# Kernel optimization log

Hardware: AMD Instinct MI355X
Metric: run time of the kernel (lower is better)

## Reference

```python
import jax, jax.numpy as jnp
import numpy as np

K = 3          # kernel size
PAD = 1        # padding


def _conv2d(x, w, b):
    # plain 3x3 conv, stride 1, pad 1, NCHW / OIHW
    out = jax.lax.conv_general_dilated(
        x, w, window_strides=(1, 1), padding=((PAD, PAD), (PAD, PAD)),
        dimension_numbers=('NCHW', 'OIHW', 'NCHW'))
    return out + b[None, :, None, None]


def _deform_conv2d(x, offsets, w, b):
    # torchvision deform_conv2d semantics (stride=1, dilation=1, no mask)
    B, C, H, W = x.shape
    K2 = K * K
    off = offsets.reshape(B, K2, 2, H, W)
    dy, dx = off[:, :, 0], off[:, :, 1]              # [B,K2,H,W], (y,x) order
    ki, kj = jnp.meshgrid(jnp.arange(K), jnp.arange(K), indexing='ij')
    ki = ki.reshape(K2).astype(x.dtype)
    kj = kj.reshape(K2).astype(x.dtype)
    base_y = (jnp.arange(H, dtype=x.dtype)[None, :, None] - PAD + ki[:, None, None])  # [K2,H,1]
    base_x = (jnp.arange(W, dtype=x.dtype)[None, None, :] - PAD + kj[:, None, None])  # [K2,1,W]
    py = base_y[None] + dy                            # [B,K2,H,W] sampling rows
    px = base_x[None] + dx                            # [B,K2,H,W] sampling cols

    y0 = jnp.floor(py); x0 = jnp.floor(px)
    y1 = y0 + 1.0;      x1 = x0 + 1.0
    wy1 = py - y0; wy0 = 1.0 - wy1
    wx1 = px - x0; wx0 = 1.0 - wx1

    def corner(yc, xc, wgt):
        valid = ((yc >= 0) & (yc <= H - 1) & (xc >= 0) & (xc <= W - 1))
        iy = jnp.clip(yc, 0, H - 1).astype(jnp.int32)
        ix = jnp.clip(xc, 0, W - 1).astype(jnp.int32)
        # per-batch gather: x[b][:, iy[b], ix[b]] -> [C,K2,H,W]
        vals = jax.vmap(lambda xb, iyb, ixb: xb[:, iyb, ixb])(x, iy, ix)
        return vals * (wgt * valid.astype(x.dtype))[:, None]  # [B,C,K2,H,W]

    sampled = (corner(y0, x0, wy0 * wx0) + corner(y0, x1, wy0 * wx1)
               + corner(y1, x0, wy1 * wx0) + corner(y1, x1, wy1 * wx1))
    out = jnp.einsum('bckhw,ock->bohw', sampled, w.reshape(w.shape[0], C, K2))
    return out + b[None, :, None, None]


def setup_inputs() -> dict:
    key = jax.random.key(0)
    ks = jax.random.split(key, 6)
    B, C, O, H, W = 4, 256, 256, 64, 64
    x = jax.random.normal(ks[0], (B, C, H, W), dtype=jnp.float32)
    y = jax.random.normal(ks[1], (B, C, H, W), dtype=jnp.float32)
    # offset conv predicts 2*K*K offset channels; small init keeps offsets a few px
    offset_w = jax.random.normal(ks[2], (2 * K * K, C, K, K), dtype=jnp.float32) * 0.01
    offset_b = jax.random.normal(ks[3], (2 * K * K,), dtype=jnp.float32) * 0.01
    deform_w = jax.random.normal(ks[4], (O, C, K, K), dtype=jnp.float32) * (1.0 / np.sqrt(C * K * K))
    deform_b = jax.random.normal(ks[5], (O,), dtype=jnp.float32) * 0.01
    return {"x": x, "y": y, "offset_w": offset_w, "offset_b": offset_b,
            "deform_w": deform_w, "deform_b": deform_b}


def reference(x, y, offset_w, offset_b, deform_w, deform_b):
    offsets = _conv2d(y, offset_w, offset_b)          # [B, 2*K*K, H, W]
    return _deform_conv2d(x, offsets, deform_w, deform_b)
```

## Files before the change

kernel.cpp:

```cpp
#include <hip/hip_runtime.h>
#include <hip/hip_bf16.h>
#include <stdint.h>


typedef __bf16 bf16x8 __attribute__((ext_vector_type(8)));
typedef float  f32x4  __attribute__((ext_vector_type(4)));

__device__ __forceinline__ unsigned short f2bfu(float f) {
    union { float f; unsigned u; } v; v.f = f;
    return (unsigned short)((v.u + 0x8000u) >> 16);
}
__device__ __forceinline__ float lo16(unsigned u) {
    union { unsigned u; float f; } v; v.u = u << 16; return v.f;
}
__device__ __forceinline__ float hi16(unsigned u) {
    union { unsigned u; float f; } v; v.u = u & 0xFFFF0000u; return v.f;
}
__device__ __forceinline__ unsigned fbits(float f) {
    union { float f; unsigned u; } v; v.f = f; return v.u;
}
__device__ __forceinline__ unsigned blend2(unsigned u0, unsigned u1, unsigned u2, unsigned u3,
                                           float4 w) {
    float lo = w.x * lo16(u0) + w.y * lo16(u1) + w.z * lo16(u2) + w.w * lo16(u3);
    float hi = w.x * hi16(u0) + w.y * hi16(u1) + w.z * hi16(u2) + w.w * hi16(u3);
    unsigned rl = fbits(lo) + 0x8000u;
    unsigned rh = fbits(hi) + 0x8000u;
    return __builtin_amdgcn_perm(rh, rl, 0x07060302);
}

__device__ __forceinline__ void wait_ge(int* f, int v) {
    while (__hip_atomic_load(f, __ATOMIC_ACQUIRE, __HIP_MEMORY_SCOPE_WORKGROUP) < v)
        __builtin_amdgcn_s_sleep(1);
}
__device__ __forceinline__ void signal_one(int* f, int lane) {
    __threadfence_block();
    if (lane == 0)
        __hip_atomic_fetch_add(f, 1, __ATOMIC_RELEASE, __HIP_MEMORY_SCOPE_WORKGROUP);
}

__global__ __launch_bounds__(256) void prep_kernel(
    const float* __restrict__ x, const float* __restrict__ y,
    const float* __restrict__ ow, const float* __restrict__ dw,
    unsigned short* __restrict__ xT, unsigned short* __restrict__ yT,
    unsigned short* __restrict__ Wp2, unsigned short* __restrict__ Bo)
{
    __shared__ float tile[64 * 69];
    int blk = blockIdx.x;
    int t = threadIdx.x;
    if (blk < 2048) {
        const float* src = x; unsigned short* dst = xT;
        if (blk >= 1024) { src = y; dst = yT; blk -= 1024; }
        int cq = blk & 3;
        int bh = blk >> 2;
        int w4 = t & 15, cl0 = t >> 4;
        const float* s = src + ((size_t)(bh >> 6) * 256 + cq * 64) * 4096 + (size_t)(bh & 63) * 64;
#pragma unroll
        for (int p = 0; p < 4; ++p) {
            int cl = p * 16 + cl0;
            float4 v = *(const float4*)&s[(size_t)cl * 4096 + w4 * 4];
            tile[(w4 * 4 + 0) * 69 + cl] = v.x;
            tile[(w4 * 4 + 1) * 69 + cl] = v.y;
            tile[(w4 * 4 + 2) * 69 + cl] = v.z;
            tile[(w4 * 4 + 3) * 69 + cl] = v.w;
        }
        __syncthreads();
        unsigned short* d = dst + (size_t)bh * 16384 + cq * 64;
#pragma unroll
        for (int p = 0; p < 4; ++p) {
            int w = p * 16 + cl0;
            float4 v = *(const float4*)&tile[w * 69 + w4 * 4];
            ushort4 r = make_ushort4(f2bfu(v.x), f2bfu(v.y), f2bfu(v.z), f2bfu(v.w));
            *(ushort4*)&d[w * 256 + w4 * 4] = r;
        }
    } else if (blk < 2336) {
        int tid = (blk - 2048) * 256 + t;
        int q8 = tid >> 8;
        int o  = tid & 255;
        int k0 = q8 * 8;
        int tap = k0 >> 8, c0 = k0 & 255;
        const float* s = dw + o * 2304 + c0 * 9 + tap;
        ushort4 r0 = make_ushort4(f2bfu(s[0]), f2bfu(s[9]), f2bfu(s[18]), f2bfu(s[27]));
        ushort4 r1 = make_ushort4(f2bfu(s[36]), f2bfu(s[45]), f2bfu(s[54]), f2bfu(s[63]));
        *(ushort4*)&Wp2[tid * 8 + 0] = r0;
        *(ushort4*)&Wp2[tid * 8 + 4] = r1;
    } else {
        int idx = (blk - 2336) * 256 + t;
        int j = idx & 7;
        int n = (idx >> 3) & 31;
        int lq = (idx >> 8) & 3;
        int kg = idx >> 10;
        int k = kg * 32 + lq * 8 + j;
        int tap = k >> 8, c = k & 255;
        float v = (n < 18) ? ow[n * 2304 + c * 9 + tap] : 0.f;
        Bo[idx] = f2bfu(v);
    }
}

__global__ __launch_bounds__(1024) void deform_kernel(
    const unsigned short* __restrict__ xT,
    const unsigned short* __restrict__ yT,
    const unsigned short* __restrict__ Wp2,
    const unsigned short* __restrict__ Bo,
    const float* __restrict__ ob,
    const float* __restrict__ db,
    float* __restrict__ out)
{
    __shared__ __align__(16) unsigned char smem[116864];
    float*  red    = (float*)smem;
    float4* pw_lds = (float4*)(smem + 98304);
    int4*   pi_lds = (int4*)(smem + 98304 + 9216);
    int*    ready  = (int*)(smem + 116736);
    int*    done   = (int*)(smem + 116736 + 36);

    int blk = blockIdx.x;
    int lb = (blk & 7) * 32 + (blk >> 3);
    int b = lb >> 6, h = lb & 63;
    int t = threadIdx.x;
    int wv = t >> 6, lane = t & 63;
    int ln = lane & 15, lq = lane >> 4;

    const unsigned short* xtb = xT + (size_t)b * (64 * 64 * 256);

    if (t < 18) ((int*)(smem + 116736))[t] = 0;

    {
        int kq = wv >> 1, mh = wv & 1;
        f32x4 oacc[2][2];
#pragma unroll
        for (int m16 = 0; m16 < 2; ++m16)
#pragma unroll
            for (int nt = 0; nt < 2; ++nt)
                oacc[m16][nt] = (f32x4){0.f, 0.f, 0.f, 0.f};
        for (int u = kq * 9; u < kq * 9 + 9; ++u) {
            int tap = u >> 3, kc = u & 7;
            int ki = tap / 3, kj = tap - ki * 3;
            int hr = h + ki - 1;
            bf16x8 b0 = *(const bf16x8*)&Bo[(tap * 8 + kc) * 1024 + lq * 256 + ln * 8];
            bf16x8 b1 = *(const bf16x8*)&Bo[(tap * 8 + kc) * 1024 + lq * 256 + (16 + ln) * 8];
#pragma unroll
            for (int m16 = 0; m16 < 2; ++m16) {
                int wr = mh * 32 + m16 * 16 + ln + kj - 1;
                bf16x8 af = (bf16x8)(__bf16)0.0f;
                if (hr >= 0 && hr < 64 && wr >= 0 && wr < 64)
                    af = *(const bf16x8*)&yT[((size_t)(b * 64 + hr) * 64 + wr) * 256 + kc * 32 + lq * 8];
                oacc[m16][0] = __builtin_amdgcn_mfma_f32_16x16x32_bf16(af, b0, oacc[m16][0], 0, 0, 0);
                oacc[m16][1] = __builtin_amdgcn_mfma_f32_16x16x32_bf16(af, b1, oacc[m16][1], 0, 0, 0);
            }
        }
        float* rz = red + (size_t)(kq * 2 + mh) * 1056;
#pragma unroll
        for (int m16 = 0; m16 < 2; ++m16)
#pragma unroll
            for (int nt = 0; nt < 2; ++nt) {
                int o_l = nt * 16 + ln;
#pragma unroll
                for (int r = 0; r < 4; ++r)
                    rz[o_l * 33 + m16 * 16 + lq * 4 + r] = oacc[m16][nt][r];
            }
    }
    __syncthreads();
    if (t < 576) {
        int tap = t >> 6, pos = t & 63;
        int mh_p = pos >> 5, pl = pos & 31;
        float dy = ob[2 * tap], dx = ob[2 * tap + 1];
#pragma unroll
        for (int kq = 0; kq < 8; ++kq) {
            const float* rz = red + (size_t)(kq * 2 + mh_p) * 1056;
            dy += rz[(2 * tap) * 33 + pl];
            dx += rz[(2 * tap + 1) * 33 + pl];
        }
        int ki = tap / 3, kj = tap - ki * 3;
        float py = (float)(h - 1 + ki) + dy;
        float px = (float)(pos - 1 + kj) + dx;
        float y0 = floorf(py), x0 = floorf(px);
        float wy1 = py - y0, wx1 = px - x0;
        float wy0 = 1.f - wy1, wx0 = 1.f - wx1;
        float y1 = y0 + 1.f, x1 = x0 + 1.f;
        float vy0 = (y0 >= 0.f && y0 <= 63.f) ? 1.f : 0.f;
        float vy1 = (y1 >= 0.f && y1 <= 63.f) ? 1.f : 0.f;
        float vx0 = (x0 >= 0.f && x0 <= 63.f) ? 1.f : 0.f;
        float vx1 = (x1 >= 0.f && x1 <= 63.f) ? 1.f : 0.f;
        int iy0 = (int)fminf(fmaxf(y0, 0.f), 63.f);
        int iy1 = (int)fminf(fmaxf(y1, 0.f), 63.f);
        int ix0 = (int)fminf(fmaxf(x0, 0.f), 63.f);
        int ix1 = (int)fminf(fmaxf(x1, 0.f), 63.f);
        pw_lds[t] = make_float4(wy0 * wx0 * vy0 * vx0, wy0 * wx1 * vy0 * vx1,
                                wy1 * wx0 * vy1 * vx0, wy1 * wx1 * vy1 * vx1);
        pi_lds[t] = make_int4((iy0 * 64 + ix0) * 256, (iy0 * 64 + ix1) * 256,
                              (iy1 * 64 + ix0) * 256, (iy1 * 64 + ix1) * 256);
    }
    __syncthreads();

    if (wv < 8) {
        int gr = lane & 31, half = lane >> 5, c0 = gr * 8;
#pragma unroll 1
        for (int tap = 0; tap < 9; ++tap) {
            if (tap >= 3) wait_ge(&done[tap - 3], 8);
            float4 gw[4]; uint4 ga[4][4];
#pragma unroll
            for (int it = 0; it < 4; ++it) {
                int pos = wv * 2 + half + it * 16;
                gw[it] = pw_lds[tap * 64 + pos];
                int4 p = pi_lds[tap * 64 + pos];
                ga[it][0] = *(const uint4*)&xtb[p.x + c0];
                ga[it][1] = *(const uint4*)&xtb[p.y + c0];
                ga[it][2] = *(const uint4*)&xtb[p.z + c0];
                ga[it][3] = *(const uint4*)&xtb[p.w + c0];
            }
            unsigned short* buf = (unsigned short*)(smem + (tap % 3) * 32768);
#pragma unroll
            for (int it = 0; it < 4; ++it) {
                int pos = wv * 2 + half + it * 16;
                uint4 res;
                res.x = blend2(ga[it][0].x, ga[it][1].x, ga[it][2].x, ga[it][3].x, gw[it]);
                res.y = blend2(ga[it][0].y, ga[it][1].y, ga[it][2].y, ga[it][3].y, gw[it]);
                res.z = blend2(ga[it][0].z, ga[it][1].z, ga[it][2].z, ga[it][3].z, gw[it]);
                res.w = blend2(ga[it][0].w, ga[it][1].w, ga[it][2].w, ga[it][3].w, gw[it]);
                *(uint4*)&buf[pos * 256 + (gr ^ (pos & 7)) * 8] = res;
            }
            signal_one(&ready[tap], lane);
        }
    } else {
        int ns = wv - 8;
        f32x4 acc[4][2];
#pragma unroll
        for (int ms = 0; ms < 4; ++ms)
#pragma unroll
            for (int nt = 0; nt < 2; ++nt)
                acc[ms][nt] = (f32x4){0.f, 0.f, 0.f, 0.f};
#pragma unroll 1
        for (int tap = 0; tap < 9; ++tap) {
            wait_ge(&ready[tap], 8);
            const unsigned short* Ab = (const unsigned short*)(smem + (tap % 3) * 32768);
#pragma unroll 2
            for (int kc = 0; kc < 8; ++kc) {
                int g = kc * 4 + lq;
                bf16x8 af[4];
#pragma unroll
                for (int ms = 0; ms < 4; ++ms) {
                    int row = ms * 16 + ln;
                    af[ms] = *(const bf16x8*)&Ab[row * 256 + (g ^ (row & 7)) * 8];
                }
                int kg = tap * 8 + kc;
                bf16x8 bfr[2];
#pragma unroll
                for (int nt = 0; nt < 2; ++nt)
                    bfr[nt] = *(const bf16x8*)&Wp2[((kg * 4 + lq) * 256 + ns * 32 + nt * 16 + ln) * 8];
#pragma unroll
                for (int ms = 0; ms < 4; ++ms)
#pragma unroll
                    for (int nt = 0; nt < 2; ++nt)
                        acc[ms][nt] = __builtin_amdgcn_mfma_f32_16x16x32_bf16(af[ms], bfr[nt], acc[ms][nt], 0, 0, 0);
            }
            signal_one(&done[tap], lane);
        }
#pragma unroll
        for (int nt = 0; nt < 2; ++nt) {
            int o = ns * 32 + nt * 16 + ln;
            float bias = db[o];
            float* ob_ptr = out + ((size_t)(b * 256 + o)) * 4096 + h * 64;
#pragma unroll
            for (int ms = 0; ms < 4; ++ms) {
                f32x4 a = acc[ms][nt];
                float4 st = make_float4(a[0] + bias, a[1] + bias, a[2] + bias, a[3] + bias);
                *(float4*)&ob_ptr[ms * 16 + lq * 4] = st;
            }
        }
    }
}

extern "C" void kernel_launch(void* const* d_in, const int* in_sizes, int n_in,
                              void* d_out, int out_size, void* d_ws, size_t ws_size,
                              hipStream_t stream) {
    const float* x  = (const float*)d_in[0];
    const float* y  = (const float*)d_in[1];
    const float* ow = (const float*)d_in[2];
    const float* ob = (const float*)d_in[3];
    const float* dw = (const float*)d_in[4];
    const float* db = (const float*)d_in[5];
    float* out = (float*)d_out;

    char* ws = (char*)d_ws;
    unsigned short* xT  = (unsigned short*)(ws);
    unsigned short* yT  = (unsigned short*)(ws + 8388608);
    unsigned short* Wp2 = (unsigned short*)(ws + 16777216);
    unsigned short* Bo  = (unsigned short*)(ws + 16777216 + 1179648);

    hipLaunchKernelGGL(prep_kernel, dim3(2624), dim3(256), 0, stream,
                       x, y, ow, dw, xT, yT, Wp2, Bo);
    hipLaunchKernelGGL(deform_kernel, dim3(256), dim3(1024), 0, stream,
                       xT, yT, Wp2, Bo, ob, db, out);
}
```

Baseline: 137.4 us.

## Split deform conv taps across two blocks per row with atomic accumulation

Each output row is now handled by two 512-thread blocks, one covering taps 0-4 and the other taps 5-8. Partial sums are combined with atomic adds into an output zeroed by a memset. The warp-specialized producer/consumer flag pipeline is replaced by a unified double-buffered loop in which every wave gathers the next tap while running MFMAs on the current one, separated by block barriers. The offset weights are repacked so each half-block only computes the offset channels for its own taps. This aims to double the number of blocks, cut LDS use per block and overlap gather with compute, at the cost of duplicated offset-conv work, atomic traffic on the output and an extra memset.

New measurement: 239.4 us. +74.3%, slower.

```diff
diff --git a/kernel.cpp b/kernel.cpp
--- a/kernel.cpp
+++ b/kernel.cpp
@@ -26,16 +26,6 @@
     unsigned rl = fbits(lo) + 0x8000u;
     unsigned rh = fbits(hi) + 0x8000u;
     return __builtin_amdgcn_perm(rh, rl, 0x07060302);
-}
-
-__device__ __forceinline__ void wait_ge(int* f, int v) {
-    while (__hip_atomic_load(f, __ATOMIC_ACQUIRE, __HIP_MEMORY_SCOPE_WORKGROUP) < v)
-        __builtin_amdgcn_s_sleep(1);
-}
-__device__ __forceinline__ void signal_one(int* f, int lane) {
-    __threadfence_block();
-    if (lane == 0)
-        __hip_atomic_fetch_add(f, 1, __ATOMIC_RELEASE, __HIP_MEMORY_SCOPE_WORKGROUP);
 }
 
 __global__ __launch_bounds__(256) void prep_kernel(
@@ -86,17 +76,20 @@
     } else {
         int idx = (blk - 2336) * 256 + t;
         int j = idx & 7;
-        int n = (idx >> 3) & 31;
+        int n32 = (idx >> 3) & 31;
         int lq = (idx >> 8) & 3;
         int kg = idx >> 10;
         int k = kg * 32 + lq * 8 + j;
-        int tap = k >> 8, c = k & 255;
-        float v = (n < 18) ? ow[n * 2304 + c * 9 + tap] : 0.f;
+        int tapk = k >> 8, c = k & 255;
+        int o = -1;
+        if (n32 < 10) o = n32;
+        else if (n32 >= 16 && n32 < 24) o = 10 + (n32 - 16);
+        float v = (o >= 0) ? ow[o * 2304 + c * 9 + tapk] : 0.f;
         Bo[idx] = f2bfu(v);
     }
 }
 
-__global__ __launch_bounds__(1024) void deform_kernel(
+__global__ __launch_bounds__(512, 4) void deform_kernel(
     const unsigned short* __restrict__ xT,
     const unsigned short* __restrict__ yT,
     const unsigned short* __restrict__ Wp2,
@@ -105,71 +98,63 @@
     const float* __restrict__ db,
     float* __restrict__ out)
 {
-    __shared__ __align__(16) unsigned char smem[116864];
+    __shared__ __align__(16) unsigned char smem[75776];
+    unsigned short* Abuf0 = (unsigned short*)smem;
+    unsigned short* Abuf1 = (unsigned short*)(smem + 32768);
     float*  red    = (float*)smem;
-    float4* pw_lds = (float4*)(smem + 98304);
-    int4*   pi_lds = (int4*)(smem + 98304 + 9216);
-    int*    ready  = (int*)(smem + 116736);
-    int*    done   = (int*)(smem + 116736 + 36);
+    float4* pw_lds = (float4*)(smem + 65536);
+    int4*   pi_lds = (int4*)(smem + 65536 + 5120);
 
     int blk = blockIdx.x;
-    int lb = (blk & 7) * 32 + (blk >> 3);
-    int b = lb >> 6, h = lb & 63;
+    int lb = (blk & 7) * 64 + (blk >> 3);
+    int b = lb >> 7, rem = lb & 127, h = rem >> 1, ks = rem & 1;
+    int tap0 = ks ? 5 : 0;
+    int ntaps = ks ? 4 : 5;
     int t = threadIdx.x;
     int wv = t >> 6, lane = t & 63;
     int ln = lane & 15, lq = lane >> 4;
 
     const unsigned short* xtb = xT + (size_t)b * (64 * 64 * 256);
 
-    if (t < 18) ((int*)(smem + 116736))[t] = 0;
-
     {
-        int kq = wv >> 1, mh = wv & 1;
-        f32x4 oacc[2][2];
-#pragma unroll
-        for (int m16 = 0; m16 < 2; ++m16)
-#pragma unroll
-            for (int nt = 0; nt < 2; ++nt)
-                oacc[m16][nt] = (f32x4){0.f, 0.f, 0.f, 0.f};
-        for (int u = kq * 9; u < kq * 9 + 9; ++u) {
-            int tap = u >> 3, kc = u & 7;
-            int ki = tap / 3, kj = tap - ki * 3;
+        f32x4 oacc[4];
+#pragma unroll
+        for (int m16 = 0; m16 < 4; ++m16) oacc[m16] = (f32x4){0.f, 0.f, 0.f, 0.f};
+        for (int u = wv * 9; u < wv * 9 + 9; ++u) {
+            int tapk = u >> 3, kc = u & 7;
+            int ki = tapk / 3, kj = tapk - ki * 3;
             int hr = h + ki - 1;
-            bf16x8 b0 = *(const bf16x8*)&Bo[(tap * 8 + kc) * 1024 + lq * 256 + ln * 8];
-            bf16x8 b1 = *(const bf16x8*)&Bo[(tap * 8 + kc) * 1024 + lq * 256 + (16 + ln) * 8];
-#pragma unroll
-            for (int m16 = 0; m16 < 2; ++m16) {
-                int wr = mh * 32 + m16 * 16 + ln + kj - 1;
+            bf16x8 bo = *(const bf16x8*)&Bo[(tapk * 8 + kc) * 1024 + lq * 256 + (ks * 16 + ln) * 8];
+#pragma unroll
+            for (int m16 = 0; m16 < 4; ++m16) {
+                int wr = m16 * 16 + ln + kj - 1;
                 bf16x8 af = (bf16x8)(__bf16)0.0f;
                 if (hr >= 0 && hr < 64 && wr >= 0 && wr < 64)
                     af = *(const bf16x8*)&yT[((size_t)(b * 64 + hr) * 64 + wr) * 256 + kc * 32 + lq * 8];
-                oacc[m16][0] = __builtin_amdgcn_mfma_f32_16x16x32_bf16(af, b0, oacc[m16][0], 0, 0, 0);
-                oacc[m16][1] = __builtin_amdgcn_mfma_f32_16x16x32_bf16(af, b1, oacc[m16][1], 0, 0, 0);
+                oacc[m16] = __builtin_amdgcn_mfma_f32_16x16x32_bf16(af, bo, oacc[m16], 0, 0, 0);
             }
         }
-        float* rz = red + (size_t)(kq * 2 + mh) * 1056;
-#pragma unroll
-        for (int m16 = 0; m16 < 2; ++m16)
-#pragma unroll
-            for (int nt = 0; nt < 2; ++nt) {
-                int o_l = nt * 16 + ln;
-#pragma unroll
-                for (int r = 0; r < 4; ++r)
-                    rz[o_l * 33 + m16 * 16 + lq * 4 + r] = oacc[m16][nt][r];
-            }
+#pragma unroll
+        for (int m16 = 0; m16 < 4; ++m16) {
+            float* rz = red + (size_t)(wv * 4 + m16) * 272;
+#pragma unroll
+            for (int r = 0; r < 4; ++r)
+                rz[ln * 17 + lq * 4 + r] = oacc[m16][r];
+        }
     }
     __syncthreads();
-    if (t < 576) {
-        int tap = t >> 6, pos = t & 63;
-        int mh_p = pos >> 5, pl = pos & 31;
-        float dy = ob[2 * tap], dx = ob[2 * tap + 1];
+    if (t < ntaps * 64) {
+        int tl = t >> 6, pos = t & 63;
+        int m16 = pos >> 4, rr = pos & 15;
+        int tapg = tap0 + tl;
+        float dy = ob[2 * tapg], dx = ob[2 * tapg + 1];
 #pragma unroll
         for (int kq = 0; kq < 8; ++kq) {
-            const float* rz = red + (size_t)(kq * 2 + mh_p) * 1056;
-            dy += rz[(2 * tap) * 33 + pl];
-            dx += rz[(2 * tap + 1) * 33 + pl];
-        }
-        int ki = tap / 3, kj = tap - ki * 3;
+            const float* rz = red + (size_t)(kq * 4 + m16) * 272;
+            dy += rz[(2 * tl) * 17 + rr];
+            dx += rz[(2 * tl + 1) * 17 + rr];
+        }
+        int ki = tapg / 3, kj = tapg - ki * 3;
         float py = (float)(h - 1 + ki) + dy;
         float px = (float)(pos - 1 + kj) + dx;
         float y0 = floorf(py), x0 = floorf(px);
@@ -191,82 +176,112 @@
     }
     __syncthreads();
 
-    if (wv < 8) {
-        int gr = lane & 31, half = lane >> 5, c0 = gr * 8;
+    int ns = wv;
+    int gr = lane & 31, c0 = gr * 8;
+    int posb = wv * 2 + (lane >> 5);
+
+    f32x4 acc[4][2];
+#pragma unroll
+    for (int ms = 0; ms < 4; ++ms)
+#pragma unroll
+        for (int nt = 0; nt < 2; ++nt)
+            acc[ms][nt] = (f32x4){0.f, 0.f, 0.f, 0.f};
+
+    uint4 ga[2][4]; float4 gw[2];
+
+#define G_ISSUE(TL, J0)                                              \
+    _Pragma("unroll")                                                \
+    for (int it = 0; it < 2; ++it) {                                 \
+        int pos = posb + ((J0) + it) * 16;                           \
+        gw[it] = pw_lds[(TL) * 64 + pos];                            \
+        int4 p = pi_lds[(TL) * 64 + pos];                            \
+        ga[it][0] = *(const uint4*)&xtb[p.x + c0];                   \
+        ga[it][1] = *(const uint4*)&xtb[p.y + c0];                   \
+        ga[it][2] = *(const uint4*)&xtb[p.z + c0];                   \
+        ga[it][3] = *(const uint4*)&xtb[p.w + c0];                   \
+    }
+#define G_COMMIT(BUF, J0)                                            \
+    _Pragma("unroll")                                                \
+    for (int it = 0; it < 2; ++it) {                                 \
+        int pos = posb + ((J0) + it) * 16;                           \
+        uint4 res;                                                   \
+        res.x = blend2(ga[it][0].x, ga[it][1].x, ga[it][2].x, ga[it][3].x, gw[it]); \
+        res.y = blend2(ga[it][0].y, ga[it][1].y, ga[it][2].y, ga[it][3].y, gw[it]); \
+        res.z = blend2(ga[it][0].z, ga[it][1].z, ga[it][2].z, ga[it][3].z, gw[it]); \
+        res.w = blend2(ga[it][0].w, ga[it][1].w, ga[it][2].w, ga[it][3].w, gw[it]); \
+        *(uint4*)&(BUF)[pos * 256 + (gr ^ (pos & 7)) * 8] = res;     \
+    }
+
+    G_ISSUE(0, 0) G_COMMIT(Abuf0, 0)
+    G_ISSUE(0, 2) G_COMMIT(Abuf0, 2)
+    __syncthreads();
+
 #pragma unroll 1
-        for (int tap = 0; tap < 9; ++tap) {
-            if (tap >= 3) wait_ge(&done[tap - 3], 8);
-            float4 gw[4]; uint4 ga[4][4];
-#pragma unroll
-            for (int it = 0; it < 4; ++it) {
-                int pos = wv * 2 + half + it * 16;
-                gw[it] = pw_lds[tap * 64 + pos];
-                int4 p = pi_lds[tap * 64 + pos];
-                ga[it][0] = *(const uint4*)&xtb[p.x + c0];
-                ga[it][1] = *(const uint4*)&xtb[p.y + c0];
-                ga[it][2] = *(const uint4*)&xtb[p.z + c0];
-                ga[it][3] = *(const uint4*)&xtb[p.w + c0];
+    for (int tl = 0; tl < ntaps; ++tl) {
+        const unsigned short* Ab = (tl & 1) ? Abuf1 : Abuf0;
+        unsigned short* Nb = (tl & 1) ? Abuf0 : Abuf1;
+        bool more = (tl + 1 < ntaps);
+        if (more) { G_ISSUE(tl + 1, 0) }
+#pragma unroll
+        for (int kc = 0; kc < 4; ++kc) {
+            int g = kc * 4 + lq;
+            bf16x8 af[4];
+#pragma unroll
+            for (int ms = 0; ms < 4; ++ms) {
+                int row = ms * 16 + ln;
+                af[ms] = *(const bf16x8*)&Ab[row * 256 + (g ^ (row & 7)) * 8];
             }
-            unsigned short* buf = (unsigned short*)(smem + (tap % 3) * 32768);
-#pragma unroll
-            for (int it = 0; it < 4; ++it) {
-                int pos = wv * 2 + half + it * 16;
-                uint4 res;
-                res.x = blend2(ga[it][0].x, ga[it][1].x, ga[it][2].x, ga[it][3].x, gw[it]);
-                res.y = blend2(ga[it][0].y, ga[it][1].y, ga[it][2].y, ga[it][3].y, gw[it]);
-                res.z = blend2(ga[it][0].z, ga[it][1].z, ga[it][2].z, ga[it][3].z, gw[it]);
-                res.w = blend2(ga[it][0].w, ga[it][1].w, ga[it][2].w, ga[it][3].w, gw[it]);
-                *(uint4*)&buf[pos * 256 + (gr ^ (pos & 7)) * 8] = res;
+            int kg = (tap0 + tl) * 8 + kc;
+            bf16x8 bfr[2];
+#pragma unroll
+            for (int nt = 0; nt < 2; ++nt)
+                bfr[nt] = *(const bf16x8*)&Wp2[((kg * 4 + lq) * 256 + ns * 32 + nt * 16 + ln) * 8];
+#pragma unroll
+            for (int ms = 0; ms < 4; ++ms)
+#pragma unroll
+                for (int nt = 0; nt < 2; ++nt)
+                    acc[ms][nt] = __builtin_amdgcn_mfma_f32_16x16x32_bf16(af[ms], bfr[nt], acc[ms][nt], 0, 0, 0);
+        }
+        if (more) { G_COMMIT(Nb, 0) G_ISSUE(tl + 1, 2) }
+#pragma unroll
+        for (int kc = 4; kc < 8; ++kc) {
+            int g = kc * 4 + lq;
+            bf16x8 af[4];
+#pragma unroll
+            for (int ms = 0; ms < 4; ++ms) {
+                int row = ms * 16 + ln;
+                af[ms] = *(const bf16x8*)&Ab[row * 256 + (g ^ (row & 7)) * 8];
             }
-            signal_one(&ready[tap], lane);
-        }
-    } else {
-        int ns = wv - 8;
-        f32x4 acc[4][2];
-#pragma unroll
-        for (int ms = 0; ms < 4; ++ms)
+            int kg = (tap0 + tl) * 8 + kc;
+            bf16x8 bfr[2];
 #pragma unroll
             for (int nt = 0; nt < 2; ++nt)
-                acc[ms][nt] = (f32x4){0.f, 0.f, 0.f, 0.f};
-#pragma unroll 1
-        for (int tap = 0; tap < 9; ++tap) {
-            wait_ge(&ready[tap], 8);
-            const unsigned short* Ab = (const unsigned short*)(smem + (tap % 3) * 32768);
-#pragma unroll 2
-            for (int kc = 0; kc < 8; ++kc) {
-                int g = kc * 4 + lq;
-                bf16x8 af[4];
-#pragma unroll
-                for (int ms = 0; ms < 4; ++ms) {
-                    int row = ms * 16 + ln;
-                    af[ms] = *(const bf16x8*)&Ab[row * 256 + (g ^ (row & 7)) * 8];
-                }
-                int kg = tap * 8 + kc;
-                bf16x8 bfr[2];
+                bfr[nt] = *(const bf16x8*)&Wp2[((kg * 4 + lq) * 256 + ns * 32 + nt * 16 + ln) * 8];
+#pragma unroll
+            for (int ms = 0; ms < 4; ++ms)
 #pragma unroll
                 for (int nt = 0; nt < 2; ++nt)
-                    bfr[nt] = *(const bf16x8*)&Wp2[((kg * 4 + lq) * 256 + ns * 32 + nt * 16 + ln) * 8];
-#pragma unroll
-                for (int ms = 0; ms < 4; ++ms)
-#pragma unroll
-                    for (int nt = 0; nt < 2; ++nt)
-                        acc[ms][nt] = __builtin_amdgcn_mfma_f32_16x16x32_bf16(af[ms], bfr[nt], acc[ms][nt], 0, 0, 0);
-            }
-            signal_one(&done[tap], lane);
-        }
-#pragma unroll
-        for (int nt = 0; nt < 2; ++nt) {
-            int o = ns * 32 + nt * 16 + ln;
-            float bias = db[o];
-            float* ob_ptr = out + ((size_t)(b * 256 + o)) * 4096 + h * 64;
-#pragma unroll
-            for (int ms = 0; ms < 4; ++ms) {
-                f32x4 a = acc[ms][nt];
-                float4 st = make_float4(a[0] + bias, a[1] + bias, a[2] + bias, a[3] + bias);
-                *(float4*)&ob_ptr[ms * 16 + lq * 4] = st;
-            }
-        }
-    }
+                    acc[ms][nt] = __builtin_amdgcn_mfma_f32_16x16x32_bf16(af[ms], bfr[nt], acc[ms][nt], 0, 0, 0);
+        }
+        if (more) { G_COMMIT(Nb, 2) }
+        __syncthreads();
+    }
+
+#pragma unroll
+    for (int nt = 0; nt < 2; ++nt) {
+        int o = ns * 32 + nt * 16 + ln;
+        float bias = ks ? 0.f : db[o];
+        float* op = out + ((size_t)(b * 256 + o)) * 4096 + h * 64;
+#pragma unroll
+        for (int ms = 0; ms < 4; ++ms) {
+            f32x4 a = acc[ms][nt];
+#pragma unroll
+            for (int r = 0; r < 4; ++r)
+                unsafeAtomicAdd(&op[ms * 16 + lq * 4 + r], a[r] + bias);
+        }
+    }
+#undef G_ISSUE
+#undef G_COMMIT
 }
 
 extern "C" void kernel_launch(void* const* d_in, const int* in_sizes, int n_in,
@@ -286,8 +301,9 @@
     unsigned short* Wp2 = (unsigned short*)(ws + 16777216);
     unsigned short* Bo  = (unsigned short*)(ws + 16777216 + 1179648);
 
+    hipMemsetAsync(out, 0, (size_t)out_size * sizeof(float), stream);
     hipLaunchKernelGGL(prep_kernel, dim3(2624), dim3(256), 0, stream,
                        x, y, ow, dw, xT, yT, Wp2, Bo);
-    hipLaunchKernelGGL(deform_kernel, dim3(256), dim3(1024), 0, stream,
+    hipLaunchKernelGGL(deform_kernel, dim3(512), dim3(512), 0, stream,
                        xT, yT, Wp2, Bo, ob, db, out);
 }
```
